# Performance work log

Hardware: AMD Instinct MI355X
Metric: run time of the kernel (lower is better)

Reference implementation:

```python
import jax, jax.numpy as jnp
import numpy as np

N_NODES = 50000
N_EDGES = 600000
NODE_DIM = 64
EDGE_DIM = 16
HIDDEN = 128
N_LAYERS = 3
N_CLASSES = 2
N_GRAPHS = 256
BN_EPS = 1e-5


def setup_inputs() -> dict:
    key = jax.random.key(0)
    ks = jax.random.split(key, 24)
    i = iter(range(24))
    def nrm(shape, scale=0.05):
        return jax.random.normal(ks[next(i)], shape, dtype=jnp.float32) * scale
    inp = {
        "x": jax.random.normal(ks[next(i)], (N_NODES, NODE_DIM), dtype=jnp.float32),
        "edge_index": jax.random.randint(ks[next(i)], (2, N_EDGES), 0, N_NODES),
        "edge_attr": jax.random.normal(ks[next(i)], (N_EDGES, EDGE_DIM), dtype=jnp.float32),
        "batch": jnp.sort(jax.random.randint(ks[next(i)], (N_NODES,), 0, N_GRAPHS)),
        # encoders
        "node_w": nrm((NODE_DIM, HIDDEN)), "node_b": jnp.zeros((HIDDEN,), jnp.float32),
        "edge_w": nrm((EDGE_DIM, HIDDEN)), "edge_b": jnp.zeros((HIDDEN,), jnp.float32),
        # per-layer GINE MLP params, stacked over layers
        "mlp_w1": nrm((N_LAYERS, HIDDEN, HIDDEN)), "mlp_b1": jnp.zeros((N_LAYERS, HIDDEN), jnp.float32),
        "mlp_w2": nrm((N_LAYERS, HIDDEN, HIDDEN)), "mlp_b2": jnp.zeros((N_LAYERS, HIDDEN), jnp.float32),
        "bn_gamma": jnp.ones((N_LAYERS, HIDDEN), jnp.float32), "bn_beta": jnp.zeros((N_LAYERS, HIDDEN), jnp.float32),
        # head
        "head_w1": nrm((HIDDEN, HIDDEN)), "head_b1": jnp.zeros((HIDDEN,), jnp.float32),
        "head_w2": nrm((HIDDEN, N_CLASSES)), "head_b2": jnp.zeros((N_CLASSES,), jnp.float32),
    }
    return inp


def _forward(x, edge_attr, node_w, node_b, edge_w, edge_b, mlp_w1, mlp_b1,
             mlp_w2, mlp_b2, bn_gamma, bn_beta, head_w1, head_b1, head_w2,
             head_b2, edge_index, batch):
    src, dst = edge_index[0], edge_index[1]
    h = x @ node_w + node_b                     # [N, H]
    ea = edge_attr @ edge_w + edge_b            # [E, H]
    for l in range(N_LAYERS):
        # GINE message: relu(x_src + edge_attr), scatter-add into dst
        msg = jax.nn.relu(h[src] + ea)          # [E, H]
        agg = jax.ops.segment_sum(msg, dst, num_segments=N_NODES)
        z = h + agg                              # (1+eps)*x + agg, eps=0
        z = jax.nn.relu(z @ mlp_w1[l] + mlp_b1[l]) @ mlp_w2[l] + mlp_b2[l]
        # BatchNorm1d over node dim (batch statistics)
        mean = jnp.mean(z, axis=0)
        var = jnp.var(z, axis=0)
        z = bn_gamma[l] * (z - mean) * jax.lax.rsqrt(var + BN_EPS) + bn_beta[l]
        h = jax.nn.relu(z)                       # dropout off (eval)
    g = jax.ops.segment_sum(h, batch, num_segments=N_GRAPHS)  # global_add_pool
    return jax.nn.relu(g @ head_w1 + head_b1) @ head_w2 + head_b2


def reference(x, edge_index, edge_attr, batch, node_w, node_b, edge_w, edge_b,
              mlp_w1, mlp_b1, mlp_w2, mlp_b2, bn_gamma, bn_beta,
              head_w1, head_b1, head_w2, head_b2):
    return _forward(x, edge_attr, node_w, node_b, edge_w, edge_b, mlp_w1,
                    mlp_b1, mlp_w2, mlp_b2, bn_gamma, bn_beta, head_w1,
                    head_b1, head_w2, head_b2, edge_index, batch)
```

## Files before the change

### kernel.cpp

```cpp
#include <hip/hip_runtime.h>

#define N_NODES_C 50000
#define N_EDGES_C 600000
#define NODE_DIM_C 64
#define EDGE_DIM_C 16
#define HID 128
#define N_GRAPHS_C 256
#define BN_EPS_C 1e-5f
#define SCAN_NBLK ((N_NODES_C + 255) / 256)

typedef short bf16x8 __attribute__((ext_vector_type(8)));
typedef float f32x4 __attribute__((ext_vector_type(4)));

__device__ __forceinline__ unsigned short f2bf(float f) {
  union { float f; unsigned u; } v; v.f = f;
  unsigned r = (v.u + 0x7fffu + ((v.u >> 16) & 1u)) >> 16;
  return (unsigned short)r;
}

__device__ __forceinline__ float2 bfp2f(unsigned u) {
  union { unsigned u; float f; } lo, hi;
  lo.u = u << 16;
  hi.u = u & 0xffff0000u;
  return make_float2(lo.f, hi.f);
}

__device__ __forceinline__ float bf2f(unsigned short s) {
  union { unsigned u; float f; } v;
  v.u = ((unsigned)s) << 16;
  return v.f;
}

__global__ __launch_bounds__(256)
void k_x2bf(const float* __restrict__ x, unsigned short* __restrict__ xb,
            int* __restrict__ cnt, float* __restrict__ g) {
  int tid = blockIdx.x * 256 + threadIdx.x;
  size_t i = (size_t)tid * 4;
  if (i < (size_t)N_NODES_C * NODE_DIM_C) {
    float4 v = *(const float4*)&x[i];
    uint2 o;
    o.x = (unsigned)f2bf(v.x) | ((unsigned)f2bf(v.y) << 16);
    o.y = (unsigned)f2bf(v.z) | ((unsigned)f2bf(v.w) << 16);
    *(uint2*)&xb[i] = o;
  }
  if (tid < N_NODES_C) cnt[tid] = 0;
  if (tid < N_GRAPHS_C * HID) g[tid] = 0.f;
}

__global__ __launch_bounds__(256)
void k_prep_w(const float* __restrict__ w1, const float* __restrict__ w2,
              const float* __restrict__ nodew, unsigned short* __restrict__ wT) {
  int m = blockIdx.x;
  if (m < 6) {
    const float* src = (m < 3) ? (w1 + (size_t)m * HID * HID)
                               : (w2 + (size_t)(m - 3) * HID * HID);
    unsigned short* dst = wT + (size_t)m * HID * HID;
    for (int i = threadIdx.x; i < HID * HID; i += 256) {
      int n = i >> 7, k = i & 127;
      dst[n * HID + k] = f2bf(src[k * HID + n]);
    }
  } else {
    unsigned short* dst = wT + (size_t)6 * HID * HID;
    for (int i = threadIdx.x; i < HID * NODE_DIM_C; i += 256) {
      int n = i >> 6, k = i & 63;
      dst[n * NODE_DIM_C + k] = f2bf(nodew[k * HID + n]);
    }
  }
}

__global__ __launch_bounds__(256)
void k_node_mfma(const unsigned short* __restrict__ xb,
                 const unsigned short* __restrict__ nwT,
                 const float* __restrict__ bias, unsigned short* __restrict__ h) {
  const int LD = NODE_DIM_C + 8;
  __shared__ unsigned short a_lds[128 * LD];
  __shared__ unsigned short w_lds[128 * LD];
  int t = threadIdx.x;
  int row0 = blockIdx.x * 128;
  {
    int r = t >> 3, c = t & 7;
#pragma unroll
    for (int it = 0; it < 4; ++it) {
      int row = it * 32 + r;
      int grow = row0 + row;
      uint4 va = (grow < N_NODES_C)
                     ? ((const uint4*)(xb + (size_t)grow * NODE_DIM_C))[c]
                     : make_uint4(0, 0, 0, 0);
      *(uint4*)&a_lds[row * LD + c * 8] = va;
      uint4 vw = ((const uint4*)(nwT + (size_t)row * NODE_DIM_C))[c];
      *(uint4*)&w_lds[row * LD + c * 8] = vw;
    }
  }
  __syncthreads();

  int lane = t & 63;
  int w = t >> 6;
  int l15 = lane & 15;
  int q = lane >> 4;

  f32x4 acc[2][8];
#pragma unroll
  for (int rt = 0; rt < 2; ++rt)
#pragma unroll
    for (int nt = 0; nt < 8; ++nt) acc[rt][nt] = (f32x4)0.f;

#pragma unroll
  for (int kk = 0; kk < 2; ++kk) {
    int k0 = kk * 32;
    bf16x8 af[2];
#pragma unroll
    for (int rt = 0; rt < 2; ++rt) {
      int arow = w * 32 + rt * 16 + l15;
      af[rt] = *(const bf16x8*)&a_lds[arow * LD + k0 + q * 8];
    }
#pragma unroll
    for (int nt = 0; nt < 8; ++nt) {
      bf16x8 bf = *(const bf16x8*)&w_lds[(nt * 16 + l15) * LD + k0 + q * 8];
#pragma unroll
      for (int rt = 0; rt < 2; ++rt)
        acc[rt][nt] = __builtin_amdgcn_mfma_f32_16x16x32_bf16(af[rt], bf, acc[rt][nt], 0, 0, 0);
    }
  }

#pragma unroll
  for (int nt = 0; nt < 8; ++nt) {
    int gcol = nt * 16 + l15;
    float bv = bias[gcol];
#pragma unroll
    for (int rt = 0; rt < 2; ++rt) {
#pragma unroll
      for (int i = 0; i < 4; ++i) {
        int grow = row0 + w * 32 + rt * 16 + q * 4 + i;
        if (grow < N_NODES_C) h[(size_t)grow * HID + gcol] = f2bf(acc[rt][nt][i] + bv);
      }
    }
  }
}

__global__ __launch_bounds__(256)
void k_histogram(const int* __restrict__ dst, int* __restrict__ counts) {
  int e = blockIdx.x * 256 + threadIdx.x;
  if (e < N_EDGES_C) atomicAdd(&counts[dst[e]], 1);
}

__global__ __launch_bounds__(256)
void k_blocksum(const int* __restrict__ cnt, int* __restrict__ partial) {
  __shared__ int ls[4];
  int t = threadIdx.x;
  int i = blockIdx.x * 256 + t;
  int v = (i < N_NODES_C) ? cnt[i] : 0;
#pragma unroll
  for (int o = 32; o > 0; o >>= 1) v += __shfl_down(v, o, 64);
  if ((t & 63) == 0) ls[t >> 6] = v;
  __syncthreads();
  if (t == 0) partial[blockIdx.x] = ls[0] + ls[1] + ls[2] + ls[3];
}

__global__ __launch_bounds__(256)
void k_scanpartials(const int* __restrict__ partial, int* __restrict__ partial_off) {
  __shared__ int s[256];
  int t = threadIdx.x;
  int v = (t < SCAN_NBLK) ? partial[t] : 0;
  s[t] = v;
  __syncthreads();
  for (int d = 1; d < 256; d <<= 1) {
    int x = (t >= d) ? s[t - d] : 0;
    __syncthreads();
    s[t] += x;
    __syncthreads();
  }
  if (t < SCAN_NBLK) partial_off[t] = s[t] - v;
}

__global__ __launch_bounds__(256)
void k_apply(int* __restrict__ cnt_cursor, const int* __restrict__ partial_off,
             int* __restrict__ row_ptr) {
  __shared__ int s[256];
  int t = threadIdx.x;
  int i = blockIdx.x * 256 + t;
  int v = (i < N_NODES_C) ? cnt_cursor[i] : 0;
  s[t] = v;
  __syncthreads();
  for (int d = 1; d < 256; d <<= 1) {
    int x = (t >= d) ? s[t - d] : 0;
    __syncthreads();
    s[t] += x;
    __syncthreads();
  }
  int excl = s[t] - v + partial_off[blockIdx.x];
  if (i < N_NODES_C) {
    row_ptr[i] = excl;
    cnt_cursor[i] = excl;
  }
  if (i == 0) row_ptr[N_NODES_C] = N_EDGES_C;
}

__global__ __launch_bounds__(256)
void k_bucket(const int* __restrict__ dst, const int* __restrict__ srcArr,
              int* __restrict__ cursor, int* __restrict__ perm,
              int* __restrict__ src_perm) {
  int e = blockIdx.x * 256 + threadIdx.x;
  if (e < N_EDGES_C) {
    int p = atomicAdd(&cursor[dst[e]], 1);
    perm[p] = e;
    src_perm[p] = srcArr[e];
  }
}

#define EE_LDW 40
#define EE_OSW 130
__global__ __launch_bounds__(256)
void k_edge_encode(const int* __restrict__ perm, const float* __restrict__ eattr,
                   const float* __restrict__ ew, const float* __restrict__ ebias,
                   unsigned short* __restrict__ ea16) {
  __shared__ unsigned short smem[128 * EE_OSW];
  unsigned short* a_lds = smem;
  unsigned short* w_lds = smem + 128 * EE_LDW;
  int t = threadIdx.x;
  int EB = blockIdx.x * 128;

  if (t < 128) {
    unsigned short tmp[16];
#pragma unroll
    for (int k = 0; k < 16; ++k) tmp[k] = f2bf(ew[k * HID + t]);
    uint4* wr = (uint4*)&w_lds[t * EE_LDW];
    wr[0] = *(uint4*)&tmp[0];
    wr[1] = *(uint4*)&tmp[8];
    wr[2] = make_uint4(0, 0, 0, 0);
    wr[3] = make_uint4(0, 0, 0, 0);
  }
  {
    int edge = t >> 1, half = t & 1;
    int gi = EB + edge;
    float4 v0 = make_float4(0, 0, 0, 0), v1 = v0;
    if (gi < N_EDGES_C) {
      int e = perm[gi];
      const float4* p = (const float4*)(eattr + (size_t)e * EDGE_DIM_C + half * 8);
      v0 = p[0];
      v1 = p[1];
    }
    unsigned short tmp[8] = {f2bf(v0.x), f2bf(v0.y), f2bf(v0.z), f2bf(v0.w),
                             f2bf(v1.x), f2bf(v1.y), f2bf(v1.z), f2bf(v1.w)};
    *(uint4*)&a_lds[edge * EE_LDW + half * 8] = *(uint4*)tmp;
    *(uint4*)&a_lds[edge * EE_LDW + 16 + half * 8] = make_uint4(0, 0, 0, 0);
  }
  __syncthreads();

  int lane = t & 63;
  int w = t >> 6;
  int l15 = lane & 15;
  int q = lane >> 4;

  f32x4 acc[2][8];
  {
    bf16x8 af[2];
#pragma unroll
    for (int rt = 0; rt < 2; ++rt) {
      int arow = w * 32 + rt * 16 + l15;
      af[rt] = *(const bf16x8*)&a_lds[arow * EE_LDW + q * 8];
    }
#pragma unroll
    for (int nt = 0; nt < 8; ++nt) {
      bf16x8 bf = *(const bf16x8*)&w_lds[(nt * 16 + l15) * EE_LDW + q * 8];
#pragma unroll
      for (int rt = 0; rt < 2; ++rt)
        acc[rt][nt] = __builtin_amdgcn_mfma_f32_16x16x32_bf16(
            af[rt], bf, (f32x4)0.f, 0, 0, 0);
    }
  }
  __syncthreads();

#pragma unroll
  for (int nt = 0; nt < 8; ++nt) {
    int col = nt * 16 + l15;
    float bv = ebias[col];
#pragma unroll
    for (int rt = 0; rt < 2; ++rt) {
#pragma unroll
      for (int i = 0; i < 4; ++i) {
        int row = w * 32 + rt * 16 + q * 4 + i;
        smem[row * EE_OSW + col] = f2bf(acc[rt][nt][i] + bv);
      }
    }
  }
  __syncthreads();

  int valid = min(128, N_EDGES_C - EB);
  for (int i = t; i < valid * 64; i += 256) {
    int row = i >> 6, c = i & 63;
    unsigned v = *(const unsigned*)&smem[row * EE_OSW + c * 2];
    *(unsigned*)&ea16[((size_t)EB + row) * HID + c * 2] = v;
  }
}

__global__ __launch_bounds__(256)
void k_aggregate(const unsigned* __restrict__ h32, const unsigned* __restrict__ ea,
                 const int* __restrict__ src_p, const int* __restrict__ row_ptr,
                 unsigned short* __restrict__ z, float* __restrict__ gsum,
                 float* __restrict__ gsumsq) {
  int t = threadIdx.x;
  if (blockIdx.x == 0 && t < HID) { gsum[t] = 0.f; gsumsq[t] = 0.f; }
  int lane = t & 63;
  int wave = t >> 6;
  int node = blockIdx.x * 4 + wave;
  if (node >= N_NODES_C) return;
  float2 base = bfp2f(h32[(size_t)node * 64 + lane]);
  float acc0 = base.x, acc1 = base.y;
  int beg = row_ptr[node], end = row_ptr[node + 1];
  int j = beg;
  for (; j + 8 <= end; j += 8) {
    int s0 = src_p[j],     s1 = src_p[j + 1], s2 = src_p[j + 2], s3 = src_p[j + 3];
    int s4 = src_p[j + 4], s5 = src_p[j + 5], s6 = src_p[j + 6], s7 = src_p[j + 7];
    unsigned g0 = h32[(size_t)s0 * 64 + lane];
    unsigned g1 = h32[(size_t)s1 * 64 + lane];
    unsigned g2 = h32[(size_t)s2 * 64 + lane];
    unsigned g3 = h32[(size_t)s3 * 64 + lane];
    unsigned g4 = h32[(size_t)s4 * 64 + lane];
    unsigned g5 = h32[(size_t)s5 * 64 + lane];
    unsigned g6 = h32[(size_t)s6 * 64 + lane];
    unsigned g7 = h32[(size_t)s7 * 64 + lane];
    unsigned u0 = ea[(size_t)j * 64 + lane];
    unsigned u1 = ea[(size_t)(j + 1) * 64 + lane];
    unsigned u2 = ea[(size_t)(j + 2) * 64 + lane];
    unsigned u3 = ea[(size_t)(j + 3) * 64 + lane];
    unsigned u4 = ea[(size_t)(j + 4) * 64 + lane];
    unsigned u5 = ea[(size_t)(j + 5) * 64 + lane];
    unsigned u6 = ea[(size_t)(j + 6) * 64 + lane];
    unsigned u7 = ea[(size_t)(j + 7) * 64 + lane];
    float2 a0 = bfp2f(g0), a1 = bfp2f(g1), a2 = bfp2f(g2), a3 = bfp2f(g3);
    float2 a4 = bfp2f(g4), a5 = bfp2f(g5), a6 = bfp2f(g6), a7 = bfp2f(g7);
    float2 e0 = bfp2f(u0), e1 = bfp2f(u1), e2 = bfp2f(u2), e3 = bfp2f(u3);
    float2 e4 = bfp2f(u4), e5 = bfp2f(u5), e6 = bfp2f(u6), e7 = bfp2f(u7);
    acc0 += fmaxf(a0.x + e0.x, 0.f) + fmaxf(a1.x + e1.x, 0.f) +
            fmaxf(a2.x + e2.x, 0.f) + fmaxf(a3.x + e3.x, 0.f) +
            fmaxf(a4.x + e4.x, 0.f) + fmaxf(a5.x + e5.x, 0.f) +
            fmaxf(a6.x + e6.x, 0.f) + fmaxf(a7.x + e7.x, 0.f);
    acc1 += fmaxf(a0.y + e0.y, 0.f) + fmaxf(a1.y + e1.y, 0.f) +
            fmaxf(a2.y + e2.y, 0.f) + fmaxf(a3.y + e3.y, 0.f) +
            fmaxf(a4.y + e4.y, 0.f) + fmaxf(a5.y + e5.y, 0.f) +
            fmaxf(a6.y + e6.y, 0.f) + fmaxf(a7.y + e7.y, 0.f);
  }
  for (; j + 4 <= end; j += 4) {
    int s0 = src_p[j], s1 = src_p[j + 1], s2 = src_p[j + 2], s3 = src_p[j + 3];
    unsigned g0 = h32[(size_t)s0 * 64 + lane];
    unsigned g1 = h32[(size_t)s1 * 64 + lane];
    unsigned g2 = h32[(size_t)s2 * 64 + lane];
    unsigned g3 = h32[(size_t)s3 * 64 + lane];
    unsigned u0 = ea[(size_t)j * 64 + lane];
    unsigned u1 = ea[(size_t)(j + 1) * 64 + lane];
    unsigned u2 = ea[(size_t)(j + 2) * 64 + lane];
    unsigned u3 = ea[(size_t)(j + 3) * 64 + lane];
    float2 a0 = bfp2f(g0), a1 = bfp2f(g1), a2 = bfp2f(g2), a3 = bfp2f(g3);
    float2 e0 = bfp2f(u0), e1 = bfp2f(u1), e2 = bfp2f(u2), e3 = bfp2f(u3);
    acc0 += fmaxf(a0.x + e0.x, 0.f) + fmaxf(a1.x + e1.x, 0.f) +
            fmaxf(a2.x + e2.x, 0.f) + fmaxf(a3.x + e3.x, 0.f);
    acc1 += fmaxf(a0.y + e0.y, 0.f) + fmaxf(a1.y + e1.y, 0.f) +
            fmaxf(a2.y + e2.y, 0.f) + fmaxf(a3.y + e3.y, 0.f);
  }
  for (; j < end; ++j) {
    int s0 = src_p[j];
    float2 a0 = bfp2f(h32[(size_t)s0 * 64 + lane]);
    float2 e0 = bfp2f(ea[(size_t)j * 64 + lane]);
    acc0 += fmaxf(a0.x + e0.x, 0.f);
    acc1 += fmaxf(a0.y + e0.y, 0.f);
  }
  unsigned packed = (unsigned)f2bf(acc0) | ((unsigned)f2bf(acc1) << 16);
  *(unsigned*)&z[(size_t)node * HID + lane * 2] = packed;
}

template <bool RELU, bool STATS>
__global__ __launch_bounds__(256)
void k_gemm_mfma(const unsigned short* __restrict__ in,
                 const unsigned short* __restrict__ wT,
                 const float* __restrict__ bias,
                 unsigned short* __restrict__ outb,
                 float* __restrict__ gsum, float* __restrict__ gsumsq) {
  const int LDA = HID + 8;
  __shared__ unsigned short a_lds[128 * LDA];
  __shared__ unsigned short w_lds[128 * LDA];
  int t = threadIdx.x;
  int row0 = blockIdx.x * 128;
  {
    int r = t >> 4, chunk = t & 15;
#pragma unroll
    for (int it = 0; it < 8; ++it) {
      int row = it * 16 + r;
      int grow = row0 + row;
      uint4 va = (grow < N_NODES_C)
                     ? ((const uint4*)(in + (size_t)grow * HID))[chunk]
                     : make_uint4(0, 0, 0, 0);
      *(uint4*)&a_lds[row * LDA + chunk * 8] = va;
      uint4 vw = ((const uint4*)(wT + (size_t)row * HID))[chunk];
      *(uint4*)&w_lds[row * LDA + chunk * 8] = vw;
    }
  }
  __syncthreads();

  int lane = t & 63;
  int w = t >> 6;
  int l15 = lane & 15;
  int q = lane >> 4;

  f32x4 acc[2][8];
#pragma unroll
  for (int rt = 0; rt < 2; ++rt)
#pragma unroll
    for (int nt = 0; nt < 8; ++nt) acc[rt][nt] = (f32x4)0.f;

#pragma unroll
  for (int kk = 0; kk < 4; ++kk) {
    int k0 = kk * 32;
    bf16x8 af[2];
#pragma unroll
    for (int rt = 0; rt < 2; ++rt) {
      int arow = w * 32 + rt * 16 + l15;
      af[rt] = *(const bf16x8*)&a_lds[arow * LDA + k0 + q * 8];
    }
#pragma unroll
    for (int nt = 0; nt < 8; ++nt) {
      int brow = nt * 16 + l15;
      bf16x8 bf = *(const bf16x8*)&w_lds[brow * LDA + k0 + q * 8];
#pragma unroll
      for (int rt = 0; rt < 2; ++rt)
        acc[rt][nt] = __builtin_amdgcn_mfma_f32_16x16x32_bf16(af[rt], bf, acc[rt][nt], 0, 0, 0);
    }
  }

  float sp[8], qp[8];
#pragma unroll
  for (int nt = 0; nt < 8; ++nt) { sp[nt] = 0.f; qp[nt] = 0.f; }

#pragma unroll
  for (int nt = 0; nt < 8; ++nt) {
    int gcol = nt * 16 + l15;
    float bv = bias[gcol];
#pragma unroll
    for (int rt = 0; rt < 2; ++rt) {
#pragma unroll
      for (int i = 0; i < 4; ++i) {
        int grow = row0 + w * 32 + rt * 16 + q * 4 + i;
        bool ok = (grow < N_NODES_C);
        float v = acc[rt][nt][i] + bv;
        if (RELU) v = fmaxf(v, 0.f);
        if (ok) outb[(size_t)grow * HID + gcol] = f2bf(v);
        if (STATS) {
          float c = ok ? v : 0.f;
          sp[nt] += c;
          qp[nt] += c * c;
        }
      }
    }
  }

  if (STATS) {
    __syncthreads();
    float* sred = (float*)a_lds;
    float* qred = sred + 128 * 16;
    int slot = w * 4 + q;
#pragma unroll
    for (int nt = 0; nt < 8; ++nt) {
      int gcol = nt * 16 + l15;
      sred[gcol * 16 + slot] = sp[nt];
      qred[gcol * 16 + slot] = qp[nt];
    }
    __syncthreads();
    if (t < 128) {
      float s = 0.f;
#pragma unroll
      for (int i = 0; i < 16; ++i) s += sred[t * 16 + i];
      atomicAdd(&gsum[t], s);
    } else {
      int f = t - 128;
      float s = 0.f;
#pragma unroll
      for (int i = 0; i < 16; ++i) s += qred[f * 16 + i];
      atomicAdd(&gsumsq[f], s);
    }
  }
}

__global__ void k_bn_finalize(const float* __restrict__ gsum, const float* __restrict__ gsumsq,
                              const float* __restrict__ gamma, const float* __restrict__ beta,
                              float* __restrict__ scale, float* __restrict__ shift) {
  int f = threadIdx.x;
  float mean = gsum[f] * (1.f / N_NODES_C);
  float var = gsumsq[f] * (1.f / N_NODES_C) - mean * mean;
  float inv = rsqrtf(var + BN_EPS_C);
  float sc = gamma[f] * inv;
  scale[f] = sc;
  shift[f] = beta[f] - mean * sc;
}

__global__ __launch_bounds__(256)
void k_bn_relu(const unsigned short* __restrict__ t2, const float* __restrict__ scale,
               const float* __restrict__ shift, unsigned short* __restrict__ h) {
  __shared__ float sc[HID], sh[HID];
  int t = threadIdx.x;
  if (t < HID) { sc[t] = scale[t]; sh[t] = shift[t]; }
  __syncthreads();
  size_t idx = ((size_t)blockIdx.x * 256 + t) * 8;
  if (idx < (size_t)N_NODES_C * HID) {
    uint4 v = *(const uint4*)&t2[idx];
    int f = (int)(idx & 127);
    float2 p0 = bfp2f(v.x), p1 = bfp2f(v.y), p2 = bfp2f(v.z), p3 = bfp2f(v.w);
    float r0 = fmaxf(p0.x * sc[f + 0] + sh[f + 0], 0.f);
    float r1 = fmaxf(p0.y * sc[f + 1] + sh[f + 1], 0.f);
    float r2 = fmaxf(p1.x * sc[f + 2] + sh[f + 2], 0.f);
    float r3 = fmaxf(p1.y * sc[f + 3] + sh[f + 3], 0.f);
    float r4 = fmaxf(p2.x * sc[f + 4] + sh[f + 4], 0.f);
    float r5 = fmaxf(p2.y * sc[f + 5] + sh[f + 5], 0.f);
    float r6 = fmaxf(p3.x * sc[f + 6] + sh[f + 6], 0.f);
    float r7 = fmaxf(p3.y * sc[f + 7] + sh[f + 7], 0.f);
    uint4 o;
    o.x = (unsigned)f2bf(r0) | ((unsigned)f2bf(r1) << 16);
    o.y = (unsigned)f2bf(r2) | ((unsigned)f2bf(r3) << 16);
    o.z = (unsigned)f2bf(r4) | ((unsigned)f2bf(r5) << 16);
    o.w = (unsigned)f2bf(r6) | ((unsigned)f2bf(r7) << 16);
    *(uint4*)&h[idx] = o;
  }
}

__global__ __launch_bounds__(128)
void k_bn_relu_pool(const unsigned short* __restrict__ t2, const float* __restrict__ scale,
                    const float* __restrict__ shift, const int* __restrict__ batch,
                    float* __restrict__ g) {
  int t = threadIdx.x;
  float sc = scale[t], sh = shift[t];
  int n0 = blockIdx.x * 64;
  if (n0 >= N_NODES_C) return;
  int end = min(n0 + 64, N_NODES_C);
  int cur = batch[n0];
  float acc = 0.f;
  for (int n = n0; n < end; ++n) {
    int b = batch[n];
    if (b != cur) {
      atomicAdd(&g[cur * HID + t], acc);
      acc = 0.f;
      cur = b;
    }
    acc += fmaxf(bf2f(t2[(size_t)n * HID + t]) * sc + sh, 0.f);
  }
  atomicAdd(&g[cur * HID + t], acc);
}

__global__ __launch_bounds__(128)
void k_head(const float* __restrict__ g, const float* __restrict__ w1,
            const float* __restrict__ b1, const float* __restrict__ w2,
            const float* __restrict__ b2, float* __restrict__ out) {
  __shared__ float gs[HID];
  __shared__ float red[HID * 2];
  int gi = blockIdx.x, t = threadIdx.x;
  gs[t] = g[gi * HID + t];
  __syncthreads();
  float acc = b1[t];
#pragma unroll 8
  for (int k = 0; k < HID; ++k) acc += gs[k] * w1[k * HID + t];
  float hid = fmaxf(acc, 0.f);
  red[t * 2] = hid * w2[t * 2];
  red[t * 2 + 1] = hid * w2[t * 2 + 1];
  __syncthreads();
  for (int s = 64; s > 0; s >>= 1) {
    if (t < s) { red[t * 2] += red[(t + s) * 2]; red[t * 2 + 1] += red[(t + s) * 2 + 1]; }
    __syncthreads();
  }
  if (t == 0) {
    out[gi * 2] = red[0] + b2[0];
    out[gi * 2 + 1] = red[1] + b2[1];
  }
}

extern "C" void kernel_launch(void* const* d_in, const int* in_sizes, int n_in,
                              void* d_out, int out_size, void* d_ws, size_t ws_size,
                              hipStream_t stream) {
  const float* x      = (const float*)d_in[0];
  const int*   eidx   = (const int*)d_in[1];
  const float* eattr  = (const float*)d_in[2];
  const int*   batch  = (const int*)d_in[3];
  const float* node_w = (const float*)d_in[4];
  const float* node_b = (const float*)d_in[5];
  const float* edge_w = (const float*)d_in[6];
  const float* edge_b = (const float*)d_in[7];
  const float* mlp_w1 = (const float*)d_in[8];
  const float* mlp_b1 = (const float*)d_in[9];
  const float* mlp_w2 = (const float*)d_in[10];
  const float* mlp_b2 = (const float*)d_in[11];
  const float* bn_g   = (const float*)d_in[12];
  const float* bn_b   = (const float*)d_in[13];
  const float* hw1    = (const float*)d_in[14];
  const float* hb1    = (const float*)d_in[15];
  const float* hw2    = (const float*)d_in[16];
  const float* hb2    = (const float*)d_in[17];
  const int* srcArr = eidx;
  const int* dstArr = eidx + N_EDGES_C;

  char* wsp = (char*)d_ws;
  size_t off = 0;
  auto alloc = [&](size_t bytes) {
    void* p = wsp + off;
    off += (bytes + 255) & ~(size_t)255;
    return p;
  };
  unsigned short* h    = (unsigned short*)alloc((size_t)N_NODES_C * HID * 2);
  unsigned short* zbf  = (unsigned short*)alloc((size_t)N_NODES_C * HID * 2);
  unsigned short* t1bf = (unsigned short*)alloc((size_t)N_NODES_C * HID * 2);
  unsigned short* t2bf = (unsigned short*)alloc((size_t)N_NODES_C * HID * 2);
  unsigned short* ea16 = (unsigned short*)alloc((size_t)N_EDGES_C * HID * 2);
  unsigned short* xb   = (unsigned short*)alloc((size_t)N_NODES_C * NODE_DIM_C * 2);
  unsigned short* wT   = (unsigned short*)alloc(((size_t)6 * HID * HID + HID * NODE_DIM_C) * 2);
  int* row_ptr   = (int*)alloc((N_NODES_C + 1) * 4);
  int* cnt_cur   = (int*)alloc(N_NODES_C * 4);
  int* perm      = (int*)alloc((size_t)N_EDGES_C * 4);
  int* src_perm  = (int*)alloc((size_t)N_EDGES_C * 4);
  int* partial   = (int*)alloc(256 * 4);
  int* partial_off = (int*)alloc(256 * 4);
  float* gsum    = (float*)alloc(HID * 4);
  float* gsumsq  = (float*)alloc(HID * 4);
  float* scale   = (float*)alloc(HID * 4);
  float* shift   = (float*)alloc(HID * 4);
  float* g       = (float*)alloc((size_t)N_GRAPHS_C * HID * 4);
  unsigned short* nwT = wT + (size_t)6 * HID * HID;

  k_x2bf<<<(N_NODES_C * NODE_DIM_C / 4 + 255) / 256, 256, 0, stream>>>(x, xb,
                                                                       cnt_cur, g);
  k_prep_w<<<7, 256, 0, stream>>>(mlp_w1, mlp_w2, node_w, wT);
  k_node_mfma<<<(N_NODES_C + 127) / 128, 256, 0, stream>>>(xb, nwT, node_b, h);
  k_histogram<<<(N_EDGES_C + 255) / 256, 256, 0, stream>>>(dstArr, cnt_cur);
  k_blocksum<<<SCAN_NBLK, 256, 0, stream>>>(cnt_cur, partial);
  k_scanpartials<<<1, 256, 0, stream>>>(partial, partial_off);
  k_apply<<<SCAN_NBLK, 256, 0, stream>>>(cnt_cur, partial_off, row_ptr);
  k_bucket<<<(N_EDGES_C + 255) / 256, 256, 0, stream>>>(dstArr, srcArr, cnt_cur,
                                                        perm, src_perm);
  k_edge_encode<<<(N_EDGES_C + 127) / 128, 256, 0, stream>>>(perm, eattr, edge_w,
                                                             edge_b, ea16);

  const int GB = (N_NODES_C + 127) / 128;
  for (int l = 0; l < 3; ++l) {
    k_aggregate<<<(N_NODES_C + 3) / 4, 256, 0, stream>>>((const unsigned*)h,
                                                         (const unsigned*)ea16,
                                                         src_perm, row_ptr, zbf,
                                                         gsum, gsumsq);
    k_gemm_mfma<true, false><<<GB, 256, 0, stream>>>(
        zbf, wT + (size_t)l * HID * HID, mlp_b1 + l * HID, t1bf, nullptr, nullptr);
    k_gemm_mfma<false, true><<<GB, 256, 0, stream>>>(
        t1bf, wT + (size_t)(3 + l) * HID * HID, mlp_b2 + l * HID, t2bf,
        gsum, gsumsq);
    k_bn_finalize<<<1, HID, 0, stream>>>(gsum, gsumsq, bn_g + l * HID, bn_b + l * HID,
                                         scale, shift);
    if (l < 2) {
      k_bn_relu<<<(N_NODES_C * HID / 8 + 255) / 256, 256, 0, stream>>>(t2bf, scale,
                                                                       shift, h);
    } else {
      k_bn_relu_pool<<<(N_NODES_C + 63) / 64, 128, 0, stream>>>(t2bf, scale, shift,
                                                                batch, g);
    }
  }
  k_head<<<N_GRAPHS_C, 128, 0, stream>>>(g, hw1, hb1, hw2, hb2, (float*)d_out);
}
```

Before: 568.0 us.

## Store encoded edge features as fp8 and fold BN finalize into apply kernels

The edge encoder now writes its output as packed fp8 (e4m3) instead of bf16, which halves the edge-feature tensor that the aggregation kernel streams on each of the three layers. The aggregation kernel decodes the pairs with the hardware fp8-to-f32 conversion. Separately, the single-block BN finalize kernel is removed and every block of the BN/ReLU kernels recomputes scale and shift from the summed statistics, saving three launches. The fp8 storage loses precision on edge embeddings, which risks accuracy tolerance.

```diff
diff --git a/kernel.cpp b/kernel.cpp
--- a/kernel.cpp
+++ b/kernel.cpp
@@ -11,6 +11,7 @@
 
 typedef short bf16x8 __attribute__((ext_vector_type(8)));
 typedef float f32x4 __attribute__((ext_vector_type(4)));
+typedef float f32x2 __attribute__((ext_vector_type(2)));
 
 __device__ __forceinline__ unsigned short f2bf(float f) {
   union { float f; unsigned u; } v; v.f = f;
@@ -29,6 +30,11 @@
   union { unsigned u; float f; } v;
   v.u = ((unsigned)s) << 16;
   return v.f;
+}
+
+__device__ __forceinline__ float2 fp8p2f(unsigned short u) {
+  f32x2 r = __builtin_amdgcn_cvt_pk_f32_fp8((int)(unsigned)u, false);
+  return make_float2(r.x, r.y);
 }
 
 __global__ __launch_bounds__(256)
@@ -208,11 +214,11 @@
 }
 
 #define EE_LDW 40
-#define EE_OSW 130
+#define EE_OSW 132
 __global__ __launch_bounds__(256)
 void k_edge_encode(const int* __restrict__ perm, const float* __restrict__ eattr,
                    const float* __restrict__ ew, const float* __restrict__ ebias,
-                   unsigned short* __restrict__ ea16) {
+                   unsigned char* __restrict__ ea8) {
   __shared__ unsigned short smem[128 * EE_OSW];
   unsigned short* a_lds = smem;
   unsigned short* w_lds = smem + 128 * EE_LDW;
@@ -286,15 +292,19 @@
   __syncthreads();
 
   int valid = min(128, N_EDGES_C - EB);
-  for (int i = t; i < valid * 64; i += 256) {
-    int row = i >> 6, c = i & 63;
-    unsigned v = *(const unsigned*)&smem[row * EE_OSW + c * 2];
-    *(unsigned*)&ea16[((size_t)EB + row) * HID + c * 2] = v;
-  }
-}
-
-__global__ __launch_bounds__(256)
-void k_aggregate(const unsigned* __restrict__ h32, const unsigned* __restrict__ ea,
+  for (int i = t; i < valid * 32; i += 256) {
+    int row = i >> 5, c = i & 31;
+    uint2 v = *(const uint2*)&smem[row * EE_OSW + c * 4];
+    float2 p0 = bfp2f(v.x);
+    float2 p1 = bfp2f(v.y);
+    int r = __builtin_amdgcn_cvt_pk_fp8_f32(p0.x, p0.y, 0, false);
+    r = __builtin_amdgcn_cvt_pk_fp8_f32(p1.x, p1.y, r, true);
+    *(unsigned*)&ea8[((size_t)EB + row) * 128 + c * 4] = (unsigned)r;
+  }
+}
+
+__global__ __launch_bounds__(256)
+void k_aggregate(const unsigned* __restrict__ h32, const unsigned char* __restrict__ ea8,
                  const int* __restrict__ src_p, const int* __restrict__ row_ptr,
                  unsigned short* __restrict__ z, float* __restrict__ gsum,
                  float* __restrict__ gsumsq) {
@@ -307,6 +317,7 @@
   float2 base = bfp2f(h32[(size_t)node * 64 + lane]);
   float acc0 = base.x, acc1 = base.y;
   int beg = row_ptr[node], end = row_ptr[node + 1];
+  const unsigned char* eap = ea8 + lane * 2;
   int j = beg;
   for (; j + 8 <= end; j += 8) {
     int s0 = src_p[j],     s1 = src_p[j + 1], s2 = src_p[j + 2], s3 = src_p[j + 3];
@@ -319,18 +330,18 @@
     unsigned g5 = h32[(size_t)s5 * 64 + lane];
     unsigned g6 = h32[(size_t)s6 * 64 + lane];
     unsigned g7 = h32[(size_t)s7 * 64 + lane];
-    unsigned u0 = ea[(size_t)j * 64 + lane];
-    unsigned u1 = ea[(size_t)(j + 1) * 64 + lane];
-    unsigned u2 = ea[(size_t)(j + 2) * 64 + lane];
-    unsigned u3 = ea[(size_t)(j + 3) * 64 + lane];
-    unsigned u4 = ea[(size_t)(j + 4) * 64 + lane];
-    unsigned u5 = ea[(size_t)(j + 5) * 64 + lane];
-    unsigned u6 = ea[(size_t)(j + 6) * 64 + lane];
-    unsigned u7 = ea[(size_t)(j + 7) * 64 + lane];
+    unsigned short u0 = *(const unsigned short*)(eap + (size_t)j * 128);
+    unsigned short u1 = *(const unsigned short*)(eap + (size_t)(j + 1) * 128);
+    unsigned short u2 = *(const unsigned short*)(eap + (size_t)(j + 2) * 128);
+    unsigned short u3 = *(const unsigned short*)(eap + (size_t)(j + 3) * 128);
+    unsigned short u4 = *(const unsigned short*)(eap + (size_t)(j + 4) * 128);
+    unsigned short u5 = *(const unsigned short*)(eap + (size_t)(j + 5) * 128);
+    unsigned short u6 = *(const unsigned short*)(eap + (size_t)(j + 6) * 128);
+    unsigned short u7 = *(const unsigned short*)(eap + (size_t)(j + 7) * 128);
     float2 a0 = bfp2f(g0), a1 = bfp2f(g1), a2 = bfp2f(g2), a3 = bfp2f(g3);
     float2 a4 = bfp2f(g4), a5 = bfp2f(g5), a6 = bfp2f(g6), a7 = bfp2f(g7);
-    float2 e0 = bfp2f(u0), e1 = bfp2f(u1), e2 = bfp2f(u2), e3 = bfp2f(u3);
-    float2 e4 = bfp2f(u4), e5 = bfp2f(u5), e6 = bfp2f(u6), e7 = bfp2f(u7);
+    float2 e0 = fp8p2f(u0), e1 = fp8p2f(u1), e2 = fp8p2f(u2), e3 = fp8p2f(u3);
+    float2 e4 = fp8p2f(u4), e5 = fp8p2f(u5), e6 = fp8p2f(u6), e7 = fp8p2f(u7);
     acc0 += fmaxf(a0.x + e0.x, 0.f) + fmaxf(a1.x + e1.x, 0.f) +
             fmaxf(a2.x + e2.x, 0.f) + fmaxf(a3.x + e3.x, 0.f) +
             fmaxf(a4.x + e4.x, 0.f) + fmaxf(a5.x + e5.x, 0.f) +
@@ -346,12 +357,12 @@
     unsigned g1 = h32[(size_t)s1 * 64 + lane];
     unsigned g2 = h32[(size_t)s2 * 64 + lane];
     unsigned g3 = h32[(size_t)s3 * 64 + lane];
-    unsigned u0 = ea[(size_t)j * 64 + lane];
-    unsigned u1 = ea[(size_t)(j + 1) * 64 + lane];
-    unsigned u2 = ea[(size_t)(j + 2) * 64 + lane];
-    unsigned u3 = ea[(size_t)(j + 3) * 64 + lane];
+    unsigned short u0 = *(const unsigned short*)(eap + (size_t)j * 128);
+    unsigned short u1 = *(const unsigned short*)(eap + (size_t)(j + 1) * 128);
+    unsigned short u2 = *(const unsigned short*)(eap + (size_t)(j + 2) * 128);
+    unsigned short u3 = *(const unsigned short*)(eap + (size_t)(j + 3) * 128);
     float2 a0 = bfp2f(g0), a1 = bfp2f(g1), a2 = bfp2f(g2), a3 = bfp2f(g3);
-    float2 e0 = bfp2f(u0), e1 = bfp2f(u1), e2 = bfp2f(u2), e3 = bfp2f(u3);
+    float2 e0 = fp8p2f(u0), e1 = fp8p2f(u1), e2 = fp8p2f(u2), e3 = fp8p2f(u3);
     acc0 += fmaxf(a0.x + e0.x, 0.f) + fmaxf(a1.x + e1.x, 0.f) +
             fmaxf(a2.x + e2.x, 0.f) + fmaxf(a3.x + e3.x, 0.f);
     acc1 += fmaxf(a0.y + e0.y, 0.f) + fmaxf(a1.y + e1.y, 0.f) +
@@ -360,7 +371,7 @@
   for (; j < end; ++j) {
     int s0 = src_p[j];
     float2 a0 = bfp2f(h32[(size_t)s0 * 64 + lane]);
-    float2 e0 = bfp2f(ea[(size_t)j * 64 + lane]);
+    float2 e0 = fp8p2f(*(const unsigned short*)(eap + (size_t)j * 128));
     acc0 += fmaxf(a0.x + e0.x, 0.f);
     acc1 += fmaxf(a0.y + e0.y, 0.f);
   }
@@ -479,24 +490,20 @@
   }
 }
 
-__global__ void k_bn_finalize(const float* __restrict__ gsum, const float* __restrict__ gsumsq,
-                              const float* __restrict__ gamma, const float* __restrict__ beta,
-                              float* __restrict__ scale, float* __restrict__ shift) {
-  int f = threadIdx.x;
-  float mean = gsum[f] * (1.f / N_NODES_C);
-  float var = gsumsq[f] * (1.f / N_NODES_C) - mean * mean;
-  float inv = rsqrtf(var + BN_EPS_C);
-  float sc = gamma[f] * inv;
-  scale[f] = sc;
-  shift[f] = beta[f] - mean * sc;
-}
-
-__global__ __launch_bounds__(256)
-void k_bn_relu(const unsigned short* __restrict__ t2, const float* __restrict__ scale,
-               const float* __restrict__ shift, unsigned short* __restrict__ h) {
+__global__ __launch_bounds__(256)
+void k_bn_relu(const unsigned short* __restrict__ t2, const float* __restrict__ gsum,
+               const float* __restrict__ gsumsq, const float* __restrict__ gamma,
+               const float* __restrict__ beta, unsigned short* __restrict__ h) {
   __shared__ float sc[HID], sh[HID];
   int t = threadIdx.x;
-  if (t < HID) { sc[t] = scale[t]; sh[t] = shift[t]; }
+  if (t < HID) {
+    float mean = gsum[t] * (1.f / N_NODES_C);
+    float var = gsumsq[t] * (1.f / N_NODES_C) - mean * mean;
+    float inv = rsqrtf(var + BN_EPS_C);
+    float s = gamma[t] * inv;
+    sc[t] = s;
+    sh[t] = beta[t] - mean * s;
+  }
   __syncthreads();
   size_t idx = ((size_t)blockIdx.x * 256 + t) * 8;
   if (idx < (size_t)N_NODES_C * HID) {
@@ -521,11 +528,16 @@
 }
 
 __global__ __launch_bounds__(128)
-void k_bn_relu_pool(const unsigned short* __restrict__ t2, const float* __restrict__ scale,
-                    const float* __restrict__ shift, const int* __restrict__ batch,
+void k_bn_relu_pool(const unsigned short* __restrict__ t2, const float* __restrict__ gsum,
+                    const float* __restrict__ gsumsq, const float* __restrict__ gamma,
+                    const float* __restrict__ beta, const int* __restrict__ batch,
                     float* __restrict__ g) {
   int t = threadIdx.x;
-  float sc = scale[t], sh = shift[t];
+  float mean = gsum[t] * (1.f / N_NODES_C);
+  float var = gsumsq[t] * (1.f / N_NODES_C) - mean * mean;
+  float inv = rsqrtf(var + BN_EPS_C);
+  float sc = gamma[t] * inv;
+  float sh = beta[t] - mean * sc;
   int n0 = blockIdx.x * 64;
   if (n0 >= N_NODES_C) return;
   int end = min(n0 + 64, N_NODES_C);
@@ -604,7 +616,7 @@
   unsigned short* zbf  = (unsigned short*)alloc((size_t)N_NODES_C * HID * 2);
   unsigned short* t1bf = (unsigned short*)alloc((size_t)N_NODES_C * HID * 2);
   unsigned short* t2bf = (unsigned short*)alloc((size_t)N_NODES_C * HID * 2);
-  unsigned short* ea16 = (unsigned short*)alloc((size_t)N_EDGES_C * HID * 2);
+  unsigned char* ea8   = (unsigned char*)alloc((size_t)N_EDGES_C * HID);
   unsigned short* xb   = (unsigned short*)alloc((size_t)N_NODES_C * NODE_DIM_C * 2);
   unsigned short* wT   = (unsigned short*)alloc(((size_t)6 * HID * HID + HID * NODE_DIM_C) * 2);
   int* row_ptr   = (int*)alloc((N_NODES_C + 1) * 4);
@@ -615,8 +627,6 @@
   int* partial_off = (int*)alloc(256 * 4);
   float* gsum    = (float*)alloc(HID * 4);
   float* gsumsq  = (float*)alloc(HID * 4);
-  float* scale   = (float*)alloc(HID * 4);
-  float* shift   = (float*)alloc(HID * 4);
   float* g       = (float*)alloc((size_t)N_GRAPHS_C * HID * 4);
   unsigned short* nwT = wT + (size_t)6 * HID * HID;
 
@@ -631,12 +641,11 @@
   k_bucket<<<(N_EDGES_C + 255) / 256, 256, 0, stream>>>(dstArr, srcArr, cnt_cur,
                                                         perm, src_perm);
   k_edge_encode<<<(N_EDGES_C + 127) / 128, 256, 0, stream>>>(perm, eattr, edge_w,
-                                                             edge_b, ea16);
+                                                             edge_b, ea8);
 
   const int GB = (N_NODES_C + 127) / 128;
   for (int l = 0; l < 3; ++l) {
-    k_aggregate<<<(N_NODES_C + 3) / 4, 256, 0, stream>>>((const unsigned*)h,
-                                                         (const unsigned*)ea16,
+    k_aggregate<<<(N_NODES_C + 3) / 4, 256, 0, stream>>>((const unsigned*)h, ea8,
                                                          src_perm, row_ptr, zbf,
                                                          gsum, gsumsq);
     k_gemm_mfma<true, false><<<GB, 256, 0, stream>>>(
@@ -644,14 +653,12 @@
     k_gemm_mfma<false, true><<<GB, 256, 0, stream>>>(
         t1bf, wT + (size_t)(3 + l) * HID * HID, mlp_b2 + l * HID, t2bf,
         gsum, gsumsq);
-    k_bn_finalize<<<1, HID, 0, stream>>>(gsum, gsumsq, bn_g + l * HID, bn_b + l * HID,
-                                         scale, shift);
     if (l < 2) {
-      k_bn_relu<<<(N_NODES_C * HID / 8 + 255) / 256, 256, 0, stream>>>(t2bf, scale,
-                                                                       shift, h);
+      k_bn_relu<<<(N_NODES_C * HID / 8 + 255) / 256, 256, 0, stream>>>(
+          t2bf, gsum, gsumsq, bn_g + l * HID, bn_b + l * HID, h);
     } else {
-      k_bn_relu_pool<<<(N_NODES_C + 63) / 64, 128, 0, stream>>>(t2bf, scale, shift,
-                                                                batch, g);
+      k_bn_relu_pool<<<(N_NODES_C + 63) / 64, 128, 0, stream>>>(
+          t2bf, gsum, gsumsq, bn_g + l * HID, bn_b + l * HID, batch, g);
     }
   }
   k_head<<<N_GRAPHS_C, 128, 0, stream>>>(g, hw1, hb1, hw2, hb2, (float*)d_out);
```

Measured after the change: 517.1 us. 1.1x faster.
